# Performance work log

Hardware: AMD Instinct MI355X
Metric: run time of the kernel (lower is better)

## Reference

```python
import jax, jax.numpy as jnp
import numpy as np

LOG2PI = float(np.log(2.0 * np.pi))
T, DZ, DX = 512, 32, 32  # dx == dz so all quad forms stack homogeneously


def _spd(key, d):
    a = jax.random.normal(key, (d, d))
    return a @ a.T / d + jnp.eye(d)


def setup_inputs() -> dict:
    key = jax.random.key(0)
    k = jax.random.split(key, 17)
    return {
        "observations": jax.random.normal(k[0], (T, DX)),
        "m_prior_mean": jax.random.normal(k[1], (DZ,)),
        "m_prior_cov": _spd(k[2], DZ),
        "m_trans_w": 0.3 * jax.random.normal(k[3], (DZ, DZ)),
        "m_trans_b": jax.random.normal(k[4], (DZ,)),
        "m_trans_cov": _spd(k[5], DZ),
        "m_emis_w": 0.3 * jax.random.normal(k[6], (DX, DZ)),
        "m_emis_b": jax.random.normal(k[7], (DX,)),
        "m_emis_cov": _spd(k[8], DX),
        "v_prior_mean": jax.random.normal(k[9], (DZ,)),
        "v_prior_cov": _spd(k[10], DZ),
        "v_trans_w": 0.3 * jax.random.normal(k[11], (DZ, DZ)),
        "v_trans_b": jax.random.normal(k[12], (DZ,)),
        "v_trans_cov": _spd(k[13], DZ),
        "v_emis_w": 0.3 * jax.random.normal(k[14], (DX, DZ)),
        "v_emis_b": jax.random.normal(k[15], (DX,)),
        "v_emis_cov": _spd(k[16], DX),
    }


def _elbo(observations, m_prior_mean, m_prior_cov, m_trans_w, m_trans_b,
          m_trans_cov, m_emis_w, m_emis_b, m_emis_cov, v_prior_mean,
          v_prior_cov, v_trans_w, v_trans_b, v_trans_cov, v_emis_w,
          v_emis_b, v_emis_cov):
    Tn, dx = observations.shape
    dz = m_trans_cov.shape[0]
    I = jnp.eye(dz, dtype=observations.dtype)

    def logdet(M):
        return jnp.log(jnp.linalg.det(M))

    def cterm(dim, ld):  # -0.5*(dim*log(2pi) + log det)
        return -0.5 * (dim * LOG2PI + ld)

    m_trans_prec = jnp.linalg.inv(m_trans_cov)
    m_trans_ld = logdet(m_trans_cov)
    m_emis_prec = jnp.linalg.inv(m_emis_cov)
    m_emis_ld = logdet(m_emis_cov)
    v_trans_prec = jnp.linalg.inv(v_trans_cov)

    # ---- Kalman filter on the variational model ----
    def kf_update(m, P, y):
        S = v_emis_w @ P @ v_emis_w.T + v_emis_cov
        K = P @ v_emis_w.T @ jnp.linalg.inv(S)
        m2 = m + K @ (y - (v_emis_w @ m + v_emis_b))
        P2 = (I - K @ v_emis_w) @ P
        return m2, P2

    def kf_step(m, P, y):
        mp = v_trans_w @ m + v_trans_b
        Pp = v_trans_w @ P @ v_trans_w.T + v_trans_cov
        return kf_update(mp, Pp, y)

    # ---- stacked quad forms; list grows by 2 per step -> 2T slots ----
    N = 2 * Tn
    Om = jnp.zeros((N, dz, dz), observations.dtype)
    A = jnp.zeros((N, dz, dz), observations.dtype)
    b = jnp.zeros((N, dz), observations.dtype)
    # slot 0: emission/obs term at t=0
    Om = Om.at[0].set(-0.5 * m_emis_prec)
    A = A.at[0].set(m_emis_w)
    b = b.at[0].set(m_emis_b - observations[0])
    # slot 1: prior term
    Om = Om.at[1].set(-0.5 * jnp.linalg.inv(m_prior_cov))
    A = A.at[1].set(I)
    b = b.at[1].set(-m_prior_mean)

    fm, fP = kf_update(v_prior_mean, v_prior_cov, observations[0])
    c0 = cterm(dz, logdet(m_prior_cov)) + cterm(dx, m_emis_ld)

    def step(carry, xs):
        fm, fP, c, Om, A, b = carry
        t, y = xs
        # backward kernel from current filtering state
        fprec = jnp.linalg.inv(fP)
        common = v_trans_w.T @ v_trans_prec
        bcov = jnp.linalg.inv(common @ v_trans_w + fprec)
        bA = bcov @ common
        ba = bcov @ (fprec @ fm - common @ v_trans_b)
        # integrate all existing quad forms under the backward kernel
        # (zero slots contribute exactly 0, so no masking is needed)
        AbC = jnp.einsum('nij,jk->nik', A, bcov)
        c = c + jnp.sum(jnp.einsum('nab,nbc,nac->n', Om, AbC, A))
        A2 = jnp.einsum('nij,jk->nik', A, bA)
        b2 = jnp.einsum('nij,j->ni', A, ba) + b
        c = c + cterm(dx, m_emis_ld) + cterm(dz, m_trans_ld)
        # transition quad form expectation constant
        c = c - 0.5 * jnp.trace(m_trans_prec @ m_trans_w @ bcov @ m_trans_w.T)
        # append obs term (slot 2t) and transition term (slot 2t+1)
        Om2 = Om.at[2 * t].set(-0.5 * m_emis_prec).at[2 * t + 1].set(-0.5 * m_trans_prec)
        A2 = A2.at[2 * t].set(m_emis_w).at[2 * t + 1].set(m_trans_w @ bA - I)
        b2 = b2.at[2 * t].set(m_emis_b - y).at[2 * t + 1].set(m_trans_w @ ba + m_trans_b)
        # backward entropy constant + 0.5*dz
        c = c - cterm(dz, logdet(bcov)) + 0.5 * dz
        fm2, fP2 = kf_step(fm, fP, y)
        return (fm2, fP2, c, Om2, A2, b2), None

    ts = jnp.arange(1, Tn)
    (fm, fP, c, Om, A, b), _ = jax.lax.scan(
        step, (fm, fP, c0, Om, A, b), (ts, observations[1:]))

    # final expectations under the filtering distribution
    c = c - cterm(dz, logdet(fP))
    # trace(Omega @ A @ fP @ A)  -- note A (not A.T), faithful to the source
    tr = jnp.einsum('nab,nbc,cd,nda->n', Om, A, fP, A)
    cm = jnp.einsum('nij,j->ni', A, fm) + b
    qf = jnp.einsum('ni,nij,nj->n', cm, Om, cm)
    c = c + jnp.sum(tr) + jnp.sum(qf) + 0.5 * dz
    return c


def reference(observations, m_prior_mean, m_prior_cov, m_trans_w, m_trans_b,
              m_trans_cov, m_emis_w, m_emis_b, m_emis_cov, v_prior_mean,
              v_prior_cov, v_trans_w, v_trans_b, v_trans_cov, v_emis_w,
              v_emis_b, v_emis_cov):
    return _elbo(observations, m_prior_mean, m_prior_cov, m_trans_w,
                 m_trans_b, m_trans_cov, m_emis_w, m_emis_b, m_emis_cov,
                 v_prior_mean, v_prior_cov, v_trans_w, v_trans_b,
                 v_trans_cov, v_emis_w, v_emis_b, v_emis_cov)
```

## Files before the change

### kernel.cpp

```cpp
#include <hip/hip_runtime.h>
#include <math.h>

#define TT 512
#define CH 8
#define NCH 64
#define NB 128
#define ST 36
#define MS 1152
#define LOG2PI 1.8378770664093453

static_assert(TT == CH * NCH, "chunking");

enum : int {
  WS_X     = 0,
  WS_BCOV  = WS_X    + TT*1024,
  WS_BA    = WS_BCOV + TT*1024,
  WS_YT    = WS_BA   + TT*32,
  WS_MTP   = WS_YT   + TT*32,
  WS_MEP   = WS_MTP + 1024,
  WS_MPP   = WS_MEP + 1024,
  WS_QI    = WS_MPP + 1024,
  WS_RI    = WS_QI  + 1024,
  WS_P0I   = WS_RI  + 1024,
  WS_QIW   = WS_P0I + 1024,
  WS_CW    = WS_QIW + 1024,
  WS_HTRI  = WS_CW  + 1024,
  WS_HTRIH = WS_HTRI+ 1024,
  WS_TQ    = WS_HTRIH+1024,
  WS_EM    = WS_TQ  + 1024,
  WS_EML   = WS_EM  + 1024,
  WS_LAM0CW= WS_EML + 1024,
  WS_QHC   = WS_LAM0CW + 1024,
  WS_C1    = WS_QHC + 1024,
  WS_EMM   = WS_C1  + 1024,
  WS_S1    = WS_EMM + 1024,
  WS_FPT   = WS_S1  + 1024,
  WS_ETA0  = WS_FPT + 1024,
  WS_CTB   = WS_ETA0 + 32,
  WS_QIVTB = WS_CTB + 32,
  WS_FMT   = WS_QIVTB + 32,
  WS_ETAF  = WS_FMT + 32,
  WS_LDS3  = WS_ETAF + 32,
  WS_DACC  = WS_LDS3 + 4,
  WS_Z512  = WS_DACC + 8,
  WS_OPS   = WS_Z512 + 1024,
  WS_GBAR  = WS_OPS + 6*3072,
  WS_ETA_A = WS_GBAR + 64,
  WS_ETA_B = WS_ETA_A + NCH*1056,
  WS_CEA   = WS_ETA_B + NCH*1056,
  WS_CEB   = WS_CEA + NCH*2048,
  WS_END   = WS_CEB + NCH*2048
};
enum : int { WS_GEA = WS_CEA, WS_GEB = WS_CEB };
static_assert(WS_DACC % 2 == 0, "double alignment");

__device__ __forceinline__ float rlane(float v, int l) {
  return __uint_as_float(__builtin_amdgcn_readlane(__float_as_uint(v), l));
}
__device__ __forceinline__ float dot4(const float4 a, const float4 b) {
  return a.x*b.x + a.y*b.y + a.z*b.z + a.w*b.w;
}

__device__ __forceinline__ double gj_inv32(float a[32]) {
  double pp = 1.0;
#pragma unroll
  for (int p = 0; p < 32; ++p) {
    const float piv = rlane(a[p], p);
    pp *= (double)piv;
    const float sc = a[p] * (1.0f / piv);
#pragma unroll
    for (int r = 0; r < 32; ++r) {
      if (r != p) a[r] -= rlane(a[r], p) * sc;
    }
    a[p] = sc;
  }
  return pp;
}

__device__ __forceinline__ double wave_inv36(float* M, int tid) {
  float a[32]; const int cc = tid & 31;
#pragma unroll
  for (int r = 0; r < 32; ++r)
    a[r] = (tid < 32) ? M[r*ST + cc] : ((r == tid - 32) ? 1.f : 0.f);
  const double pp = gj_inv32(a);
  if (tid >= 32) {
    const int c2 = tid - 32;
#pragma unroll
// ... 83 lines not shown
  const int ri = tid >> 3, j4 = (tid & 7) * 4;
  float4 acc = *(const float4*)(Base + ri*ST + j4);
#pragma unroll 8
  for (int k = 0; k < 32; ++k) {
    const float a = A[ri*ST + k];
    const float4 b = *(const float4*)(B + k*ST + j4);
    acc.x -= a*b.x; acc.y -= a*b.y; acc.z -= a*b.z; acc.w -= a*b.w;
  }
  *(float4*)(C + ri*ST + j4) = acc;
}
__device__ __forceinline__ void mm_tp(const float* A, const float* B, float* C, int tid) {
  const int ri = tid >> 3, j4 = (tid & 7) * 4;
  float4 acc = {0.f,0.f,0.f,0.f};
#pragma unroll 8
  for (int k = 0; k < 32; ++k) {
    const float a = A[k*ST + ri];
    const float4 b = *(const float4*)(B + k*ST + j4);
    acc.x += a*b.x; acc.y += a*b.y; acc.z += a*b.z; acc.w += a*b.w;
  }
  *(float4*)(C + ri*ST + j4) = acc;
}
__device__ __forceinline__ void mm_tp_addL(const float* A, const float* B,
                                           const float* AddL, float* C, int tid) {
  const int ri = tid >> 3, j4 = (tid & 7) * 4;
  float4 acc = *(const float4*)(AddL + ri*ST + j4);
#pragma unroll 8
  for (int k = 0; k < 32; ++k) {
    const float a = A[k*ST + ri];
    const float4 b = *(const float4*)(B + k*ST + j4);
    acc.x += a*b.x; acc.y += a*b.y; acc.z += a*b.z; acc.w += a*b.w;
  }
  *(float4*)(C + ri*ST + j4) = acc;
}
__device__ __forceinline__ void mm_tp_addg(const float* A, const float* B,
                                           const float* __restrict__ gAdd,
                                           float* C, int tid) {
  const int ri = tid >> 3, j4 = (tid & 7) * 4;
  float4 acc = *(const float4*)(gAdd + ri*32 + j4);
#pragma unroll 8
  for (int k = 0; k < 32; ++k) {
    const float a = A[k*ST + ri];
    const float4 b = *(const float4*)(B + k*ST + j4);
    acc.x += a*b.x; acc.y += a*b.y; acc.z += a*b.z; acc.w += a*b.w;
  }
  *(float4*)(C + ri*ST + j4) = acc;
}

__device__ __forceinline__ void gridbar(unsigned* bars, int idx) {
  __syncthreads();
  if (threadIdx.x == 0) {
    __threadfence();
    __hip_atomic_fetch_add(&bars[idx], 1u, __ATOMIC_RELEASE, __HIP_MEMORY_SCOPE_AGENT);
    while (__hip_atomic_load(&bars[idx], __ATOMIC_ACQUIRE, __HIP_MEMORY_SCOPE_AGENT)
           < (unsigned)NB)
      __builtin_amdgcn_s_sleep(2);
  }
  __syncthreads();
}

__device__ void dev_k2(const float* __restrict__ obs, const float* __restrict__ vpm,
                       const float* __restrict__ vtw, const float* __restrict__ vtb,
                       const float* __restrict__ vew, const float* __restrict__ veb,
                       const float* __restrict__ mtw, const float* __restrict__ mew,
                       float* __restrict__ ws, int tid) {
  const int j = tid & 31, r0 = tid >> 5;
#pragma unroll
  for (int m = 0; m < 4; ++m) {
    const int ri = r0 + 8*m;
    float s1 = 0.f, s2 = 0.f, s3 = 0.f, s4 = 0.f;
    for (int k = 0; k < 32; ++k) {
      s1 += ws[WS_QI  + ri*32 + k] * vtw[k*32 + j];
      s2 += vew[k*32 + ri] * ws[WS_RI + k*32 + j];
      s3 += ws[WS_MTP + ri*32 + k] * mtw[k*32 + j];
      s4 += ws[WS_MEP + ri*32 + k] * mew[k*32 + j];
    }
    ws[WS_QIW + ri*32 + j] = s1;
    ws[WS_HTRI + ri*32 + j] = s2;
    ws[WS_FPT + ri*32 + j] = s3;
    ws[WS_EML + ri*32 + j] = -0.5f * s4;
  }
  __syncthreads();
#pragma unroll
  for (int m = 0; m < 4; ++m) {
    const int ri = r0 + 8*m;
    float s1 = 0.f, s2 = 0.f, s3 = 0.f, s4 = 0.f;
    for (int k = 0; k < 32; ++k) {
      s1 += vtw[k*32 + ri] * ws[WS_QIW + k*32 + j];
      s2 += ws[WS_HTRI + ri*32 + k] * vew[k*32 + j];
// ... 5 lines not shown
    ws[WS_LAM0CW + ri*32 + j] = ws[WS_P0I + ri*32 + j] + s1 + s2;
    ws[WS_QHC    + ri*32 + j] = ws[WS_QI  + ri*32 + j] + s1 + s2;
    ws[WS_TQ + ri*32 + j] = s3;
    ws[WS_EM + ri*32 + j] = s4;
    ws[WS_S1 + ri*32 + j] = s4 - 0.5f * ws[WS_MPP + ri*32 + j];
    ws[WS_C1 + ri*32 + j] = ws[WS_FPT + j*32 + ri];
    ws[WS_EMM + ri*32 + j] = s4 - 0.5f * ws[WS_MTP + ri*32 + j];
  }
  if (tid < 32) {
    float s1 = 0.f, s2 = 0.f, s3 = 0.f;
    for (int k = 0; k < 32; ++k) {
      s1 += ws[WS_QIW + k*32 + tid] * vtb[k];
      s2 += ws[WS_P0I + tid*32 + k] * vpm[k]
          + ws[WS_HTRI + tid*32 + k] * (obs[k] - veb[k]);
      s3 += ws[WS_QI + tid*32 + k] * vtb[k];
    }
    ws[WS_CTB + tid] = s1;
    ws[WS_ETA0 + tid] = s2;
    ws[WS_QIVTB + tid] = s3;
  }
  __syncthreads();
  if (tid == 0) {
    const double ldmt = (double)ws[WS_LDS3 + 0];
    const double ldme = (double)ws[WS_LDS3 + 1];
    const double ldmp = (double)ws[WS_LDS3 + 2];
    const double ct_me = -0.5 * (32.0 * LOG2PI + ldme);
    const double ct_mt = -0.5 * (32.0 * LOG2PI + ldmt);
    const double ct_mp = -0.5 * (32.0 * LOG2PI + ldmp);
    double c = ct_mp + ct_me;
    c += (double)(TT - 1) * (ct_me + ct_mt + 0.5 * 32.0 * LOG2PI + 16.0);
    c += 0.5 * 32.0 * LOG2PI + 16.0;
    ((double*)(ws + WS_DACC))[0] = c;
  }
}

__device__ void dev_compose(float* __restrict__ ws, float* sm, int tid) {
  float *Kc = sm,      *Ac = sm+MS,   *Gc = sm+2*MS;
  float *Kn = sm+3*MS, *An = sm+4*MS, *Gn = sm+5*MS;
  float *Mi = sm+6*MS, *V1 = sm+7*MS, *Wm = sm+8*MS;
  stage_mat(ws + WS_QHC, Kc, tid);
  stage_mat(ws + WS_QIW, Ac, tid);
  for (int e = tid; e < MS; e += 256) Gc[e] = 0.f;
  __syncthreads();
  for (int d = 0; d < 8; ++d) {
    for (int e = tid; e < MS; e += 256) Mi[e] = Kc[e] + Gc[e];
    __syncthreads();
    if (tid < 64) wave_inv36(Mi, tid);
    __syncthreads();
    mm_rr(Ac, Mi, V1, tid);
    mm_tp(Ac, Mi, Wm, tid);
    __syncthreads();
    mm_rr_sub(V1, Ac, Kc, Kn, tid);
    mm_p(V1, Ac, An, tid);
    mm_p_sub(Wm, Ac, Gc, Gn, tid);
    __syncthreads();
    float* tp;
    tp=Kc; Kc=Kn; Kn=tp;  tp=Ac; Ac=An; An=tp;  tp=Gc; Gc=Gn; Gn=tp;
    if (d >= 2) {
      float* op = ws + WS_OPS + (d-2)*3072;
      destage_mat(Kc, op, tid);
      destage_mat(Ac, op + 1024, tid);
      destage_mat(Gc, op + 2048, tid);
    }
  }
}

__device__ void dev_keta_a(float* __restrict__ ws, float* sm, int tid, int c) {
  float *Aa = sm, *Ab = sm+MS, *Xl = sm+2*MS, *bb = sm+3*MS;
  const int t1 = CH*c + 1;
  stage_mat(ws + WS_X + t1*1024, Aa, tid);
  if (tid < 32) bb[tid] = ws[WS_YT + t1*32 + tid];
  __syncthreads();
  float *Acur = Aa, *Anew = Ab; int pb = 0;
  for (int t = t1 + 1; t <= t1 + CH - 1; ++t) {
    stage_mat(ws + WS_X + t*1024, Xl, tid);
    __syncthreads();
    mm_p(Xl, Acur, Anew, tid);
    if (tid < 32) {
      float s = ws[WS_YT + t*32 + tid];
      for (int k = 0; k < 32; ++k) s += Xl[tid*ST+k] * bb[pb*32 + k];
      bb[(pb^1)*32 + tid] = s;
    }
    __syncthreads();
    float* tp = Acur; Acur = Anew; Anew = tp; pb ^= 1;
  }
  float* dst = ws + WS_ETA_A + (c+1)*1056;
  destage_mat(Acur, dst, tid);
  if (tid < 32) dst[1024 + tid] = bb[pb*32 + tid];
}

__device__ void dev_eta_lvl4(float* __restrict__ ws, float* sm,
                             int inoff, int outoff, int step, int tid, int c) {
  const float* in = ws + inoff;
  float* out = ws + outoff;
  float *AR0 = sm, *AR1 = sm+MS, *A0 = sm+2*MS;
  float *bv = sm+3*MS;
  float *b0 = bv + 64;
  stage_mat(in + c*1056, AR0, tid);
  if (tid < 32) bv[tid] = in[c*1056 + 1024 + tid];
  __syncthreads();
  float *AR = AR0, *At = AR1; int pb = 0;
  for (int kk = 1; kk <= 3; ++kk) {
    const int idx = c - kk*step;
    if (idx < 0) break;
    stage_mat(in + idx*1056, A0, tid);
    if (tid < 32) b0[tid] = in[idx*1056 + 1024 + tid];
    __syncthreads();
    mm_p(AR, A0, At, tid);
    if (tid < 32) {
      float s = bv[pb*32 + tid];
      for (int k = 0; k < 32; ++k) s += AR[tid*ST+k] * b0[k];
      bv[(pb^1)*32 + tid] = s;
    }
    __syncthreads();
    float* tp = AR; AR = At; At = tp; pb ^= 1;
  }
  destage_mat(AR, out + c*1056, tid);
  if (tid < 32) out[c*1056 + 1024 + tid] = bv[pb*32 + tid];
}

__device__ void dev_keta_b(float* __restrict__ ws, float* sm, int tid, int c) {
  float *Ap = sm, *Bl = sm+MS, *Xl = sm+2*MS, *zeta = sm+3*MS, *zn = zeta+32;
  const int nst = (c == NCH-1) ? CH-1 : CH;
  stage_mat(ws + WS_ETA_B + c*1056, Ap, tid);
  __syncthreads();
  if (tid < 32) {
    float s = ws[WS_ETA_B + c*1056 + 1024 + tid];
    for (int k = 0; k < 32; ++k)
      s += Ap[tid*ST+k] * (ws[WS_ETA0 + k] - ws[WS_CTB + k]);
    zeta[tid] = s;
  }
  __syncthreads();
  for (int i = 0; i < nst; ++i) {
    const int t = CH*c + 1 + i;
    stage_mat(ws + WS_BCOV + t*1024, Bl, tid);
    stage_mat(ws + WS_X + t*1024, Xl, tid);
    __syncthreads();
    if (tid < 32) {
      float s = 0.f;
      for (int k = 0; k < 32; ++k) s += Bl[tid*ST+k] * zeta[k];
      ws[WS_BA + t*32 + tid] = s;
    } else if (tid < 64) {
      const int i2 = tid - 32;
      float s = ws[WS_YT + t*32 + i2];
      for (int k = 0; k < 32; ++k) s += Xl[i2*ST+k] * zeta[k];
      zn[i2] = s;
    }
    __syncthreads();
    if (tid < 32) zeta[tid] = zn[tid];
    __syncthreads();
  }
  if (c == NCH-1 && tid < 32)
    ws[WS_ETAF + tid] = zeta[tid] + ws[WS_CTB + tid];
}

__device__ void dev_ksa(float* __restrict__ ws, float* sm, int tid, int c) {
  float *BTa=sm,      *BTb=sm+MS,   *Ka=sm+2*MS,  *Kb=sm+3*MS,
        *Tk=sm+4*MS,  *XC1=sm+5*MS, *Xl=sm+6*MS,  *KmTQ=sm+7*MS,
        *TQl=sm+8*MS, *EMMl=sm+9*MS,*C1l=sm+10*MS;
  const int t1 = CH*c + 1, t2 = CH*c + CH;
  const int j = tid & 31, r0 = tid >> 5;
  stage_mat(ws + WS_TQ, TQl, tid);
  stage_mat(ws + WS_EMM, EMMl, tid);
  stage_mat(ws + WS_C1, C1l, tid);
  for (int e = tid; e < MS; e += 256) {
// ... 4 lines not shown
  __syncthreads();
  float *BTc = BTa, *BTn = BTb, *Kc = Ka, *Kn = Kb;
  for (int t = t1; t <= t2; ++t) {
    stage_mat(ws + WS_X + t*1024, Xl, tid);
    for (int e = tid; e < MS; e += 256) KmTQ[e] = Kc[e] - 0.5f * TQl[e];
    __syncthreads();
    mm_rr(BTc, Xl, BTn, tid);
    mm_rr(Xl, KmTQ, Tk, tid);
    mm_p(Xl, C1l, XC1, tid);
    __syncthreads();
    {
      float4 xb[8];
#pragma unroll
      for (int kk = 0; kk < 8; ++kk) xb[kk] = *(const float4*)(Xl + j*ST + 4*kk);
#pragma unroll
      for (int m = 0; m < 4; ++m) {
        const int ri = r0 + 8*m;
        float s = 0.f;
#pragma unroll
        for (int kk = 0; kk < 8; ++kk)
          s += dot4(*(const float4*)(Tk + ri*ST + 4*kk), xb[kk]);
        Kn[ri*ST+j] = s + 0.5f*(XC1[ri*ST+j] + XC1[j*ST+ri]) + EMMl[ri*ST+j];
      }
    }
    __syncthreads();
    float* tp = BTc; BTc = BTn; BTn = tp;
    tp = Kc; Kc = Kn; Kn = tp;
  }
  float* dst = ws + WS_CEA + (c+1)*2048;
  destage_mat(BTc, dst, tid);
  destage_mat(Kc, dst + 1024, tid);
}

__device__ void dev_ks_lvl4(float* __restrict__ ws, float* sm,
                            int inoff, int outoff, int step, int tid, int c) {
  const float* in = ws + inoff;
  float* out = ws + outoff;
  float *BT0=sm,      *BT1=sm+MS,   *K0=sm+2*MS, *K1=sm+3*MS,
        *BTo=sm+4*MS, *Ko=sm+5*MS,  *tmp=sm+6*MS;
  stage_mat(in + c*2048, BT0, tid);
  stage_mat(in + c*2048 + 1024, K0, tid);
  __syncthreads();
  float *BTR = BT0, *BTt = BT1, *KR = K0, *Kt = K1;
  for (int kk = 1; kk <= 3; ++kk) {
    const int idx = c - kk*step;
    if (idx < 0) break;
    stage_mat(in + idx*2048, BTo, tid);
    stage_mat(in + idx*2048 + 1024, Ko, tid);
    __syncthreads();
    mm_p(Ko, BTR, tmp, tid);
    mm_p(BTo, BTR, BTt, tid);
    __syncthreads();
    mm_tp_addL(BTR, tmp, KR, Kt, tid);
    __syncthreads();
    float* tp = BTR; BTR = BTt; BTt = tp;
    tp = KR; KR = Kt; Kt = tp;
  }
  destage_mat(BTR, out + c*2048, tid);
  destage_mat(KR, out + c*2048 + 1024, tid);
}

__device__ void dev_ksc(float* __restrict__ ws, float* sm, float* red,
                        int tid, int c) {
  float *TQl=sm,    *EMMl=sm+MS,  *C1l=sm+2*MS, *BTP=sm+3*MS, *T1=sm+4*MS,
        *S=sm+5*MS, *SmTQ=sm+6*MS,*Xl=sm+7*MS,  *Bcl=sm+8*MS, *XC1=sm+9*MS;
  const int j = tid & 31, r0 = tid >> 5;
  stage_mat(ws + WS_TQ, TQl, tid);
  stage_mat(ws + WS_EMM, EMMl, tid);
  stage_mat(ws + WS_C1, C1l, tid);
  stage_mat(ws + WS_CEB + c*2048, BTP, tid);
  stage_mat(ws + WS_S1, SmTQ, tid);
  __syncthreads();
  mm_p(SmTQ, BTP, T1, tid);
  __syncthreads();
  mm_tp_addg(BTP, T1, ws + WS_CEB + c*2048 + 1024, S, tid);
  __syncthreads();
  double accd = 0.0;
  for (int i = 0; i < CH; ++i) {
    const int t = CH*c + 1 + i;
    if (t >= TT) break;
    stage_mat(ws + WS_X + t*1024, Xl, tid);
    stage_mat(ws + WS_BCOV + t*1024, Bcl, tid);
#pragma unroll
    for (int m = 0; m < 4; ++m) {
      const int ri = r0 + 8*m;
      SmTQ[ri*ST+j] = S[ri*ST+j] - 0.5f * TQl[ri*ST+j];
    }
    __syncthreads();
    float part = 0.f;
#pragma unroll
    for (int m = 0; m < 4; ++m) {
      const int ri = r0 + 8*m;
      part += SmTQ[ri*ST+j] * Bcl[ri*ST+j];
    }
    const float r2 = block_reduce(part, red, tid);
    if (tid == 0) accd += (double)r2;
    mm_rr(Xl, SmTQ, T1, tid);
    mm_p(Xl, C1l, XC1, tid);
    __syncthreads();
    {
      float4 xb[8];
#pragma unroll
      for (int kk = 0; kk < 8; ++kk) xb[kk] = *(const float4*)(Xl + j*ST + 4*kk);
#pragma unroll
      for (int m = 0; m < 4; ++m) {
        const int ri = r0 + 8*m;
        float s = 0.f;
#pragma unroll
        for (int kk = 0; kk < 8; ++kk)
          s += dot4(*(const float4*)(T1 + ri*ST + 4*kk), xb[kk]);
        S[ri*ST+j] = s + 0.5f*(XC1[ri*ST+j] + XC1[j*ST+ri]) + EMMl[ri*ST+j];
      }
    }
    __syncthreads();
  }
  if (tid == 0) atomicAdd(((double*)(ws + WS_DACC)) + 2, accd);
}

__device__ void dev_kga(float* __restrict__ ws, float* sm, int tid, int c) {
  float *ATa = sm, *ATb = sm+MS, *Xl = sm+2*MS, *bb = sm+3*MS;
  const int t1 = CH*c + 1;
  const int t2 = (CH*c + CH < TT) ? CH*c + CH : TT - 1;
  stage_mat(ws + WS_X + t2*1024, ATa, tid);
  if (tid < 32) bb[tid] = ws[WS_BA + t2*32 + tid];
  __syncthreads();
  float *ATc = ATa, *ATn = ATb;
  int pb = 0;
  for (int t = t2 - 1; t >= t1; --t) {
    stage_mat(ws + WS_X + t*1024, Xl, tid);
    __syncthreads();
    mm_p(ATc, Xl, ATn, tid);
    if (tid < 32) {
      float s = ws[WS_BA + t*32 + tid];
      for (int k = 0; k < 32; ++k) s += Xl[k*ST+tid] * bb[pb*32 + k];
      bb[(pb^1)*32 + tid] = s;
    }
    __syncthreads();
    float* tp = ATc; ATc = ATn; ATn = tp; pb ^= 1;
  }
  float* dst = ws + WS_GEA + (c-1)*1056;
  destage_mat(ATc, dst, tid);
  if (tid < 32) dst[1024 + tid] = bb[pb*32 + tid];
}

__device__ void dev_kg_lvl4(float* __restrict__ ws, float* sm,
                            int inoff, int outoff, int step, int tid, int c) {
  const float* in = ws + inoff;
  float* out = ws + outoff;
  float *AR0 = sm, *AR1 = sm+MS, *ATl = sm+2*MS;
  float *bv = sm+3*MS, *bl = bv + 64;
  stage_mat(in + c*1056, AR0, tid);
  if (tid < 32) bv[tid] = in[c*1056 + 1024 + tid];
  __syncthreads();
  float *AR = AR0, *At = AR1; int pb = 0;
  for (int kk = 1; kk <= 3; ++kk) {
    const int idx = c + kk*step;
    if (idx > NCH - 1) break;
    stage_mat(in + idx*1056, ATl, tid);
    if (tid < 32) bl[tid] = in[idx*1056 + 1024 + tid];
    __syncthreads();
    mm_p(ATl, AR, At, tid);
    if (tid < 32) {
      float s = bv[pb*32 + tid];
      for (int k = 0; k < 32; ++k) s += AR[k*ST+tid] * bl[k];
      bv[(pb^1)*32 + tid] = s;
    }
    __syncthreads();
    float* tp = AR; AR = At; At = tp; pb ^= 1;
  }
  destage_mat(AR, out + c*1056, tid);
  if (tid < 32) out[c*1056 + 1024 + tid] = bv[pb*32 + tid];
}

__device__ void dev_kgb(const float* __restrict__ obs, const float* __restrict__ mpm,
                        const float* __restrict__ mtw, const float* __restrict__ mtb,
                        const float* __restrict__ mew, const float* __restrict__ meb,
                        float* __restrict__ ws, float* sm, float* red, int tid, int c) {
  float *ATa=sm,      *ATb=sm+MS,    *Xl=sm+2*MS,  *Y1=sm+3*MS,  *Y2=sm+4*MS,
        *Jb=sm+5*MS,  *M2T=sm+6*MS,  *mewl=sm+7*MS,*EmLl=sm+8*MS,
        *fPl=sm+9*MS, *Mtpl=sm+10*MS,*Mepl=sm+11*MS,*mtwl=sm+12*MS;
  float *vec = sm + 13*MS;
  float *fml=vec, *mebl=vec+32, *mtbl=vec+64, *mpml=vec+96, *yl=vec+128,
        *bal=vec+160, *gv=vec+192, *cme=vec+224, *cmo=vec+256, *bv=vec+288;
  const int j = tid & 31, r0 = tid >> 5;
  stage_mat(mew, mewl, tid);
  stage_mat(ws + WS_EML, EmLl, tid);
  stage_mat(ws + WS_FPT, fPl, tid);
  stage_mat(ws + WS_MTP, Mtpl, tid);
  stage_mat(ws + WS_MEP, Mepl, tid);
  stage_mat(mtw, mtwl, tid);
  stage_mat(ws + WS_GEB + c*1056, ATa, tid);
  if (tid < 32) {
    fml[tid] = ws[WS_FMT + tid];
    mebl[tid] = meb[tid]; mtbl[tid] = mtb[tid]; mpml[tid] = mpm[tid];
    bv[tid] = ws[WS_GEB + c*1056 + 1024 + tid];
  }
  __syncthreads();
  float *ATc = ATa, *ATo = ATb;
  int bc = 0;
  double accd = 0.0;
  for (int s = CH*c + CH - 1; s >= CH*c; --s) {
    if (s < TT-1) stage_mat(ws + WS_X + (s+1)*1024, Xl, tid);
    if (s == 0)   stage_mat(ws + WS_MPP, Jb, tid);
    if (tid < 32) {
      yl[tid] = obs[s*32 + tid];
      if (s >= 1) bal[tid] = ws[WS_BA + s*32 + tid];
    }
    __syncthreads();
    if (s < TT-1) {
      mm_p(ATc, Xl, ATo, tid);
      if (tid < 32) {
        float v = ws[WS_BA + (s+1)*32 + tid];
        for (int k = 0; k < 32; ++k) v += Xl[k*ST+tid] * bv[bc*32 + k];
        bv[(bc^1)*32 + tid] = v;
      }
    }
    __syncthreads();
    const float* AT = (s < TT-1) ? ATo : ATc;
    const float* bl = (s < TT-1) ? (bv + (bc^1)*32) : (bv + bc*32);
    mm_rr(mewl, AT, Y1, tid);
    mm_rr(EmLl, AT, Y2, tid);
    if (s >= 1) {
      const float* Xg = ws + WS_X + s*1024;
      float4 xg[8];
#pragma unroll
      for (int kk = 0; kk < 8; ++kk) xg[kk] = *(const float4*)(Xg + j*32 + 4*kk);
#pragma unroll
      for (int m = 0; m < 4; ++m) {
        const int ri = r0 + 8*m;
        float v = 0.f;
#pragma unroll
        for (int kk = 0; kk < 8; ++kk)
// ... 22 lines not shown
      }
      cmo[tid] = s2v;
    }
    __syncthreads();
    const float* M2Tp = (s >= 1) ? M2T : AT;
    const float* Mqp  = (s >= 1) ? Mtpl : Jb;
    float4 fb[8], m2b[8];
#pragma unroll
    for (int kk = 0; kk < 8; ++kk) {
      fb[kk]  = *(const float4*)(fPl + j*ST + 4*kk);
      m2b[kk] = *(const float4*)(M2Tp + j*ST + 4*kk);
    }
    float part = 0.f;
#pragma unroll
    for (int m = 0; m < 4; ++m) {
      const int ri = r0 + 8*m;
      float y3 = 0.f, e2 = 0.f, e1 = 0.f;
#pragma unroll
      for (int kk = 0; kk < 8; ++kk) {
        y3 += dot4(*(const float4*)(Y2 + ri*ST + 4*kk), fb[kk]);
        e2 += dot4(fb[kk], *(const float4*)(M2Tp + ri*ST + 4*kk));
        e1 += dot4(*(const float4*)(Mqp + ri*ST + 4*kk), m2b[kk]);
      }
      part += y3 * Y1[j*ST+ri]
            - 0.5f * e1 * e2
            - 0.5f * cme[ri] * Mepl[ri*ST+j] * cme[j]
            - 0.5f * cmo[ri] * Mqp[ri*ST+j] * cmo[j];
    }
    const float r2 = block_reduce(part, red, tid);
    if (tid == 0) accd += (double)r2;
    if (s < TT-1) { float* tp = ATc; ATc = ATo; ATo = tp; bc ^= 1; }
    __syncthreads();
  }
  if (tid == 0) atomicAdd(((double*)(ws + WS_DACC)) + 3, accd);
}

__global__ __launch_bounds__(128) void k0_init(float* __restrict__ ws) {
  const int tid = threadIdx.x;
  if (tid < 64) ((unsigned*)(ws + WS_GBAR))[tid] = 0u;
  if (tid == 64) ((double*)(ws + WS_DACC))[1] = 0.0;
  if (tid == 65) ((double*)(ws + WS_DACC))[2] = 0.0;
  if (tid == 66) ((double*)(ws + WS_DACC))[3] = 0.0;
}

__global__ __launch_bounds__(256) void mega(
    const float* __restrict__ obs, const float* __restrict__ mpm,
    const float* __restrict__ mpc, const float* __restrict__ mtw,
    const float* __restrict__ mtb, const float* __restrict__ mtc,
    const float* __restrict__ mew, const float* __restrict__ meb,
    const float* __restrict__ mec, const float* __restrict__ vpm,
    const float* __restrict__ vpc, const float* __restrict__ vtw,
    const float* __restrict__ vtb, const float* __restrict__ vtc,
    const float* __restrict__ vew, const float* __restrict__ veb,
    const float* __restrict__ vcc, float* __restrict__ ws,
    float* __restrict__ out) {
  __shared__ __align__(16) float sm[15360];
  __shared__ float red[4];
  const int tid = threadIdx.x, blk = blockIdx.x;
  unsigned* bars = (unsigned*)(ws + WS_GBAR);
  int bix = 0;

  if (blk < 6) {
    const float* src = blk==0?mtc : blk==1?mec : blk==2?mpc : blk==3?vtc : blk==4?vcc : vpc;
    float* dst = ws + (blk==0?WS_MTP : blk==1?WS_MEP : blk==2?WS_MPP :
                       blk==3?WS_QI  : blk==4?WS_RI  : WS_P0I);
    if (tid < 64) {
      float a[32]; const int cc = tid & 31;
#pragma unroll
      for (int r = 0; r < 32; ++r)
        a[r] = (tid < 32) ? src[r*32 + cc] : ((r == tid - 32) ? 1.f : 0.f);
      const double pp = gj_inv32(a);
      if (tid >= 32) {
        const int c2 = tid - 32;
#pragma unroll
        for (int r = 0; r < 32; ++r) dst[r*32 + c2] = a[r];
      }
      if (tid == 0 && blk < 3) ws[WS_LDS3 + blk] = (float)log(pp);
    }
  }
  gridbar(bars, bix++);

  if (blk == 0) dev_k2(obs, vpm, vtw, vtb, vew, veb, mtw, mew, ws, tid);
  gridbar(bars, bix++);

  if (blk == 0) {
    dev_compose(ws, sm, tid);
  } else if (blk <= NCH) {
    const int tb = blk - 1;
    const int t = tb*CH + (tid >> 5), i = tid & 31;
    float s = ws[WS_QIVTB + i] - ws[WS_CTB + i];
    for (int k = 0; k < 32; ++k)
      s += ws[WS_HTRI + i*32 + k] * (obs[t*32 + k] - veb[k]);
    ws[WS_YT + t*32 + i] = s;
  }
  gridbar(bars, bix++);

  if (blk < NCH) {
    float *Zl=sm, *Mi=sm+MS, *Aol=sm+2*MS, *V1=sm+3*MS;
    float *Bcv=sm+4*MS, *Xs=sm+5*MS, *QiWl=sm+6*MS, *QHCl=sm+7*MS;
    const int c = blk;
    stage_mat(ws + WS_LAM0CW, Zl, tid);
    stage_mat(ws + WS_QIW, QiWl, tid);
    stage_mat(ws + WS_QHC, QHCl, tid);
    __syncthreads();
    for (int k = 0; k < 6; ++k) {
      if (!((c >> k) & 1)) continue;
      const float* OP = ws + WS_OPS + k*3072;
      {
        const int r = tid >> 3, c4 = (tid & 7) * 4;
        const float4 g = *(const float4*)(OP + 2048 + r*32 + c4);
        float4 z = *(const float4*)(Zl + r*ST + c4);
        z.x += g.x; z.y += g.y; z.z += g.z; z.w += g.w;
        *(float4*)(Mi + r*ST + c4) = z;
      }
      stage_mat(OP + 1024, Aol, tid);
      __syncthreads();
      if (tid < 64) wave_inv36(Mi, tid);
      __syncthreads();
      mm_rr(Aol, Mi, V1, tid);
      __syncthreads();
      mm_rr_subg(V1, Aol, OP, Zl, tid);
      __syncthreads();
    }
    const int nst = (c == NCH-1) ? CH-1 : CH;
    double acc = 0.0;
    for (int i = 0; i < nst; ++i) {
      const int t = CH*c + 1 + i;
      if (tid < 64) {
        float a[32]; const int cc = tid & 31;
#pragma unroll
        for (int r = 0; r < 32; ++r)
          a[r] = (tid < 32) ? Zl[r*ST+cc] : ((r == tid - 32) ? 1.f : 0.f);
        const double pp = gj_inv32(a);
        if (tid >= 32) {
          const int c2 = tid - 32;
#pragma unroll
          for (int r = 0; r < 32; ++r) {
            Bcv[r*ST + c2] = a[r];
            ws[WS_BCOV + t*1024 + r*32 + c2] = a[r];
          }
        }
        if (tid == 0) acc += -log(pp);
      }
      __syncthreads();
      mm_rr(QiWl, Bcv, Xs, tid);
      __syncthreads();
      destage_mat(Xs, ws + WS_X + t*1024, tid);
      mm_rr_sub(Xs, QiWl, QHCl, Zl, tid);
      __syncthreads();
    }
    if (c == NCH-1) destage_mat(Zl, ws + WS_Z512, tid);
    if (tid == 0) atomicAdd(((double*)(ws + WS_DACC)) + 1, acc);
  }
  gridbar(bars, bix++);

  if (blk < NCH) {
    if (blk < NCH-1) {
      dev_keta_a(ws, sm, tid, blk);
    } else {
      for (int e = tid; e < 1056; e += 256)
        ws[WS_ETA_A + e] = (e < 1024 && ((e >> 5) == (e & 31))) ? 1.f : 0.f;
    }
  } else {
    const int c = blk - NCH;
    if (c < NCH-1) {
      dev_ksa(ws, sm, tid, c);
    } else {
      for (int e = tid; e < 2048; e += 256)
        ws[WS_CEA + e] = (e < 1024 && ((e >> 5) == (e & 31))) ? 1.f : 0.f;
    }
  }
  gridbar(bars, bix++);

  {
    const int steps[3] = {1, 4, 16};
#pragma unroll
    for (int L = 0; L < 3; ++L) {
      const int inA = (L & 1) == 0;
      if (blk < NCH) {
        dev_eta_lvl4(ws, sm, inA ? WS_ETA_A : WS_ETA_B,
                     inA ? WS_ETA_B : WS_ETA_A, steps[L], tid, blk);
      } else {
        dev_ks_lvl4(ws, sm, inA ? WS_CEA : WS_CEB,
                    inA ? WS_CEB : WS_CEA, steps[L], tid, blk - NCH);
      }
      gridbar(bars, bix++);
    }
  }

  if (blk < NCH) {
    dev_keta_b(ws, sm, tid, blk);
    __threadfence();
    __syncthreads();
    if (blk == 0) {
      for (int e = tid; e < 1056; e += 256)
        ws[WS_GEA + (NCH-1)*1056 + e] =
            (e < 1024 && ((e >> 5) == (e & 31))) ? 1.f : 0.f;
    } else {
      dev_kga(ws, sm, tid, blk);
    }
  } else {
    dev_ksc(ws, sm, red, tid, blk - NCH);
  }
  gridbar(bars, bix++);

  {
    const int steps[3] = {1, 4, 16};
#pragma unroll
    for (int L = 0; L < 3; ++L) {
      const int inA = (L & 1) == 0;
      if (blk < NCH) {
        dev_kg_lvl4(ws, sm, inA ? WS_GEA : WS_GEB,
                    inA ? WS_GEB : WS_GEA, steps[L], tid, blk);
      } else if (L == 0 && blk == NB-1) {
        if (tid < 64) {
          float a[32]; const int cc = tid & 31;
#pragma unroll
          for (int r = 0; r < 32; ++r) {
            const float v = ws[WS_Z512 + r*32 + cc] - ws[WS_CW + r*32 + cc];
            a[r] = (tid < 32) ? v : ((r == tid - 32) ? 1.f : 0.f);
          }
          const double pp = gj_inv32(a);
          if (tid >= 32) {
            const int c2 = tid - 32;
            float fmv = 0.f;
#pragma unroll
            for (int r = 0; r < 32; ++r) {
              ws[WS_FPT + r*32 + c2] = a[r];
              fmv += a[r] * ws[WS_ETAF + r];
            }
            ws[WS_FMT + c2] = fmv;
          }
          if (tid == 0) {
            double* d = (double*)(ws + WS_DACC);
            d[1] = 0.5 * (d[1] + (-log(pp)));
          }
        }
      }
      gridbar(bars, bix++);
    }
  }

  if (blk < NCH) dev_kgb(obs, mpm, mtw, mtb, mew, meb, ws, sm, red, tid, blk);
  gridbar(bars, bix++);

  if (blk == 0 && tid == 0) {
    const double* d = (const double*)(ws + WS_DACC);
    out[0] = (float)(d[0] + d[1] + d[2] + d[3]);
  }
}

extern "C" void kernel_launch(void* const* d_in, const int* in_sizes, int n_in,
                              void* d_out, int out_size, void* d_ws, size_t ws_size,
                              hipStream_t stream) {
  (void)in_sizes; (void)n_in; (void)out_size; (void)ws_size;
  const float* obs = (const float*)d_in[0];
  const float* mpm = (const float*)d_in[1];
  const float* mpc = (const float*)d_in[2];
  const float* mtw = (const float*)d_in[3];
  const float* mtb = (const float*)d_in[4];
  const float* mtc = (const float*)d_in[5];
  const float* mew = (const float*)d_in[6];
  const float* meb = (const float*)d_in[7];
  const float* mec = (const float*)d_in[8];
  const float* vpm = (const float*)d_in[9];
  const float* vpc = (const float*)d_in[10];
  const float* vtw = (const float*)d_in[11];
  const float* vtb = (const float*)d_in[12];
  const float* vtc = (const float*)d_in[13];
  const float* vew = (const float*)d_in[14];
  const float* veb = (const float*)d_in[15];
  const float* vcc = (const float*)d_in[16];
  float* ws  = (float*)d_ws;
  float* out = (float*)d_out;

  k0_init<<<1, 128, 0, stream>>>(ws);
  mega<<<NB, 256, 0, stream>>>(obs, mpm, mpc, mtw, mtb, mtc, mew, meb, mec,
                               vpm, vpc, vtw, vtb, vtc, vew, veb, vcc, ws, out);
}
```

Before: 618.5 us.

## Cut grid barriers with hierarchical barrier, radix-8 scans, and per-block partial sums

Replaces the three radix-4 parallel-scan levels (step 1,4,16) with one radix-8 level plus a stride-8 second pass folded into the following consumer stages, dropping four grid barriers in each scan. Merges the k2 and compose stages and moves the Y-transform onto idle blocks, removing two more barriers. The grid barrier becomes a two-level group/global tree with separate cache-line-spaced counters. Double atomicAdd accumulations become per-block partial slots reduced by a final shuffle. The cost is more serial matmuls per block in each scan stage, traded for fewer global synchronisations.

```diff
diff --git a/kernel.cpp b/kernel.cpp
--- a/kernel.cpp
+++ b/kernel.cpp
@@ -5,6 +5,8 @@
 #define CH 8
 #define NCH 64
 #define NB 128
+#define NGRP 8
+#define GSZ (NB/NGRP)
 #define ST 36
 #define MS 1152
 #define LOG2PI 1.8378770664093453
@@ -45,14 +47,14 @@
   WS_Z512  = WS_DACC + 8,
   WS_OPS   = WS_Z512 + 1024,
   WS_GBAR  = WS_OPS + 6*3072,
-  WS_ETA_A = WS_GBAR + 64,
+  WS_PART  = WS_GBAR + 4352,
+  WS_ETA_A = WS_PART + 416,
   WS_ETA_B = WS_ETA_A + NCH*1056,
   WS_CEA   = WS_ETA_B + NCH*1056,
   WS_CEB   = WS_CEA + NCH*2048,
   WS_END   = WS_CEB + NCH*2048
 };
-enum : int { WS_GEA = WS_CEA, WS_GEB = WS_CEB };
-static_assert(WS_DACC % 2 == 0, "double alignment");
+static_assert(WS_DACC % 2 == 0 && WS_PART % 2 == 0, "double alignment");
 
 __device__ __forceinline__ float rlane(float v, int l) {
   return __uint_as_float(__builtin_amdgcn_readlane(__float_as_uint(v), l));
@@ -202,28 +204,29 @@
   }
   *(float4*)(C + ri*ST + j4) = acc;
 }
-__device__ __forceinline__ void mm_tp_addg(const float* A, const float* B,
-                                           const float* __restrict__ gAdd,
-                                           float* C, int tid) {
-  const int ri = tid >> 3, j4 = (tid & 7) * 4;
-  float4 acc = *(const float4*)(gAdd + ri*32 + j4);
-#pragma unroll 8
-  for (int k = 0; k < 32; ++k) {
-    const float a = A[k*ST + ri];
-    const float4 b = *(const float4*)(B + k*ST + j4);
-    acc.x += a*b.x; acc.y += a*b.y; acc.z += a*b.z; acc.w += a*b.w;
-  }
-  *(float4*)(C + ri*ST + j4) = acc;
-}
-
-__device__ __forceinline__ void gridbar(unsigned* bars, int idx) {
+
+__device__ __forceinline__ void gridbar(unsigned* base, int idx, int blk) {
   __syncthreads();
   if (threadIdx.x == 0) {
+    const int g = blk & (NGRP-1);
+    unsigned* lcl  = base + idx*128 + g*16;
+    unsigned* go   = base + 2048 + idx*128 + g*16;
+    unsigned* glob = base + 4096 + idx*16;
     __threadfence();
-    __hip_atomic_fetch_add(&bars[idx], 1u, __ATOMIC_RELEASE, __HIP_MEMORY_SCOPE_AGENT);
-    while (__hip_atomic_load(&bars[idx], __ATOMIC_ACQUIRE, __HIP_MEMORY_SCOPE_AGENT)
-           < (unsigned)NB)
-      __builtin_amdgcn_s_sleep(2);
+    __hip_atomic_fetch_add(lcl, 1u, __ATOMIC_RELEASE, __HIP_MEMORY_SCOPE_AGENT);
+    if (blk < NGRP) {
+      while (__hip_atomic_load(lcl, __ATOMIC_ACQUIRE, __HIP_MEMORY_SCOPE_AGENT)
+             < (unsigned)GSZ)
+        __builtin_amdgcn_s_sleep(1);
+      __hip_atomic_fetch_add(glob, 1u, __ATOMIC_RELEASE, __HIP_MEMORY_SCOPE_AGENT);
+      while (__hip_atomic_load(glob, __ATOMIC_ACQUIRE, __HIP_MEMORY_SCOPE_AGENT)
+             < (unsigned)NGRP)
+        __builtin_amdgcn_s_sleep(1);
+      __hip_atomic_store(go, 1u, __ATOMIC_RELEASE, __HIP_MEMORY_SCOPE_AGENT);
+    } else {
+      while (__hip_atomic_load(go, __ATOMIC_ACQUIRE, __HIP_MEMORY_SCOPE_AGENT) == 0u)
+        __builtin_amdgcn_s_sleep(1);
+    }
   }
   __syncthreads();
 }
@@ -295,6 +298,7 @@
     c += 0.5 * 32.0 * LOG2PI + 16.0;
     ((double*)(ws + WS_DACC))[0] = c;
   }
+  __syncthreads();
 }
 
 __device__ void dev_compose(float* __restrict__ ws, float* sm, int tid) {
@@ -352,19 +356,17 @@
   if (tid < 32) dst[1024 + tid] = bb[pb*32 + tid];
 }
 
-__device__ void dev_eta_lvl4(float* __restrict__ ws, float* sm,
-                             int inoff, int outoff, int step, int tid, int c) {
-  const float* in = ws + inoff;
-  float* out = ws + outoff;
+__device__ void dev_eta_lvl8(float* __restrict__ ws, float* sm, int tid, int c) {
+  const float* in = ws + WS_ETA_A;
+  float* out = ws + WS_ETA_B;
   float *AR0 = sm, *AR1 = sm+MS, *A0 = sm+2*MS;
-  float *bv = sm+3*MS;
-  float *b0 = bv + 64;
+  float *bv = sm+3*MS, *b0 = bv + 64;
   stage_mat(in + c*1056, AR0, tid);
   if (tid < 32) bv[tid] = in[c*1056 + 1024 + tid];
   __syncthreads();
   float *AR = AR0, *At = AR1; int pb = 0;
-  for (int kk = 1; kk <= 3; ++kk) {
-    const int idx = c - kk*step;
+  for (int kk = 1; kk <= 7; ++kk) {
+    const int idx = c - kk;
     if (idx < 0) break;
     stage_mat(in + idx*1056, A0, tid);
     if (tid < 32) b0[tid] = in[idx*1056 + 1024 + tid];
@@ -383,17 +385,37 @@
 }
 
 __device__ void dev_keta_b(float* __restrict__ ws, float* sm, int tid, int c) {
-  float *Ap = sm, *Bl = sm+MS, *Xl = sm+2*MS, *zeta = sm+3*MS, *zn = zeta+32;
+  float *A_0 = sm, *A_1 = sm+MS, *A_2 = sm+2*MS;
+  float *bb = sm+3*MS;
+  stage_mat(ws + WS_ETA_B + c*1056, A_0, tid);
+  if (tid < 32) bb[tid] = ws[WS_ETA_B + c*1056 + 1024 + tid];
+  __syncthreads();
+  float *AR = A_0, *Ax = A_1; int pb = 0;
+  for (int kk = 1; kk <= 7; ++kk) {
+    const int idx = c - 8*kk;
+    if (idx < 0) break;
+    stage_mat(ws + WS_ETA_B + idx*1056, A_2, tid);
+    if (tid < 32) bb[64 + tid] = ws[WS_ETA_B + idx*1056 + 1024 + tid];
+    __syncthreads();
+    mm_p(AR, A_2, Ax, tid);
+    if (tid < 32) {
+      float s = bb[pb*32 + tid];
+      for (int k = 0; k < 32; ++k) s += AR[tid*ST+k] * bb[64+k];
+      bb[(pb^1)*32 + tid] = s;
+    }
+    __syncthreads();
+    float* tp = AR; AR = Ax; Ax = tp; pb ^= 1;
+  }
+  float *zeta = bb + 96, *zn = bb + 128;
+  if (tid < 32) {
+    float s = bb[pb*32 + tid];
+    for (int k = 0; k < 32; ++k)
+      s += AR[tid*ST+k] * (ws[WS_ETA0 + k] - ws[WS_CTB + k]);
+    zeta[tid] = s;
+  }
+  __syncthreads();
+  float *Bl = A_0, *Xl = A_1;
   const int nst = (c == NCH-1) ? CH-1 : CH;
-  stage_mat(ws + WS_ETA_B + c*1056, Ap, tid);
-  __syncthreads();
-  if (tid < 32) {
-    float s = ws[WS_ETA_B + c*1056 + 1024 + tid];
-    for (int k = 0; k < 32; ++k)
-      s += Ap[tid*ST+k] * (ws[WS_ETA0 + k] - ws[WS_CTB + k]);
-    zeta[tid] = s;
-  }
-  __syncthreads();
   for (int i = 0; i < nst; ++i) {
     const int t = CH*c + 1 + i;
     stage_mat(ws + WS_BCOV + t*1024, Bl, tid);
@@ -464,18 +486,17 @@
   destage_mat(Kc, dst + 1024, tid);
 }
 
-__device__ void dev_ks_lvl4(float* __restrict__ ws, float* sm,
-                            int inoff, int outoff, int step, int tid, int c) {
-  const float* in = ws + inoff;
-  float* out = ws + outoff;
-  float *BT0=sm,      *BT1=sm+MS,   *K0=sm+2*MS, *K1=sm+3*MS,
-        *BTo=sm+4*MS, *Ko=sm+5*MS,  *tmp=sm+6*MS;
+__device__ void dev_ks_lvl8(float* __restrict__ ws, float* sm, int tid, int c) {
+  const float* in = ws + WS_CEA;
+  float* out = ws + WS_CEB;
+  float *BT0=sm, *BT1=sm+MS, *K0=sm+2*MS, *K1=sm+3*MS,
+        *BTo=sm+4*MS, *Ko=sm+5*MS, *tmp=sm+6*MS;
   stage_mat(in + c*2048, BT0, tid);
   stage_mat(in + c*2048 + 1024, K0, tid);
   __syncthreads();
-  float *BTR = BT0, *BTt = BT1, *KR = K0, *Kt = K1;
-  for (int kk = 1; kk <= 3; ++kk) {
-    const int idx = c - kk*step;
+  float *BTR=BT0, *BTt=BT1, *KR=K0, *Kt=K1;
+  for (int kk = 1; kk <= 7; ++kk) {
+    const int idx = c - kk;
     if (idx < 0) break;
     stage_mat(in + idx*2048, BTo, tid);
     stage_mat(in + idx*2048 + 1024, Ko, tid);
@@ -494,18 +515,38 @@
 
 __device__ void dev_ksc(float* __restrict__ ws, float* sm, float* red,
                         int tid, int c) {
-  float *TQl=sm,    *EMMl=sm+MS,  *C1l=sm+2*MS, *BTP=sm+3*MS, *T1=sm+4*MS,
-        *S=sm+5*MS, *SmTQ=sm+6*MS,*Xl=sm+7*MS,  *Bcl=sm+8*MS, *XC1=sm+9*MS;
+  float *BT0=sm, *BT1=sm+MS, *K0=sm+2*MS, *K1=sm+3*MS,
+        *BTo=sm+4*MS, *Ko=sm+5*MS, *tmp=sm+6*MS;
+  stage_mat(ws + WS_CEB + c*2048, BT0, tid);
+  stage_mat(ws + WS_CEB + c*2048 + 1024, K0, tid);
+  __syncthreads();
+  float *BTR=BT0, *BTt=BT1, *KR=K0, *Kt=K1;
+  for (int kk = 1; kk <= 7; ++kk) {
+    const int idx = c - 8*kk;
+    if (idx < 0) break;
+    stage_mat(ws + WS_CEB + idx*2048, BTo, tid);
+    stage_mat(ws + WS_CEB + idx*2048 + 1024, Ko, tid);
+    __syncthreads();
+    mm_p(Ko, BTR, tmp, tid);
+    mm_p(BTo, BTR, BTt, tid);
+    __syncthreads();
+    mm_tp_addL(BTR, tmp, KR, Kt, tid);
+    __syncthreads();
+    float* tp = BTR; BTR = BTt; BTt = tp;
+    tp = KR; KR = Kt; Kt = tp;
+  }
+  float *TQl=sm+7*MS, *EMMl=sm+8*MS, *C1l=sm+9*MS,
+        *S=sm+10*MS, *SmTQ=sm+11*MS, *XC1=sm+12*MS;
+  float *T1=tmp, *Xl=BTo, *Bcl=Ko;
   const int j = tid & 31, r0 = tid >> 5;
   stage_mat(ws + WS_TQ, TQl, tid);
   stage_mat(ws + WS_EMM, EMMl, tid);
   stage_mat(ws + WS_C1, C1l, tid);
-  stage_mat(ws + WS_CEB + c*2048, BTP, tid);
   stage_mat(ws + WS_S1, SmTQ, tid);
   __syncthreads();
-  mm_p(SmTQ, BTP, T1, tid);
-  __syncthreads();
-  mm_tp_addg(BTP, T1, ws + WS_CEB + c*2048 + 1024, S, tid);
+  mm_p(SmTQ, BTR, T1, tid);
+  __syncthreads();
+  mm_tp_addL(BTR, T1, KR, S, tid);
   __syncthreads();
   double accd = 0.0;
   for (int i = 0; i < CH; ++i) {
@@ -546,7 +587,7 @@
     }
     __syncthreads();
   }
-  if (tid == 0) atomicAdd(((double*)(ws + WS_DACC)) + 2, accd);
+  if (tid == 0) ((double*)(ws + WS_PART))[64 + c] = accd;
 }
 
 __device__ void dev_kga(float* __restrict__ ws, float* sm, int tid, int c) {
@@ -570,23 +611,22 @@
     __syncthreads();
     float* tp = ATc; ATc = ATn; ATn = tp; pb ^= 1;
   }
-  float* dst = ws + WS_GEA + (c-1)*1056;
+  float* dst = ws + WS_CEA + (c-1)*1056;
   destage_mat(ATc, dst, tid);
   if (tid < 32) dst[1024 + tid] = bb[pb*32 + tid];
 }
 
-__device__ void dev_kg_lvl4(float* __restrict__ ws, float* sm,
-                            int inoff, int outoff, int step, int tid, int c) {
-  const float* in = ws + inoff;
-  float* out = ws + outoff;
+__device__ void dev_kg_lvl8(float* __restrict__ ws, float* sm, int tid, int c) {
+  const float* in = ws + WS_CEA;
+  float* out = ws + WS_CEB;
   float *AR0 = sm, *AR1 = sm+MS, *ATl = sm+2*MS;
   float *bv = sm+3*MS, *bl = bv + 64;
   stage_mat(in + c*1056, AR0, tid);
   if (tid < 32) bv[tid] = in[c*1056 + 1024 + tid];
   __syncthreads();
   float *AR = AR0, *At = AR1; int pb = 0;
-  for (int kk = 1; kk <= 3; ++kk) {
-    const int idx = c + kk*step;
+  for (int kk = 1; kk <= 7; ++kk) {
+    const int idx = c + kk;
     if (idx > NCH - 1) break;
     stage_mat(in + idx*1056, ATl, tid);
     if (tid < 32) bl[tid] = in[idx*1056 + 1024 + tid];
@@ -621,15 +661,30 @@
   stage_mat(ws + WS_MTP, Mtpl, tid);
   stage_mat(ws + WS_MEP, Mepl, tid);
   stage_mat(mtw, mtwl, tid);
-  stage_mat(ws + WS_GEB + c*1056, ATa, tid);
+  stage_mat(ws + WS_CEB + c*1056, ATa, tid);
   if (tid < 32) {
     fml[tid] = ws[WS_FMT + tid];
     mebl[tid] = meb[tid]; mtbl[tid] = mtb[tid]; mpml[tid] = mpm[tid];
-    bv[tid] = ws[WS_GEB + c*1056 + 1024 + tid];
+    bv[tid] = ws[WS_CEB + c*1056 + 1024 + tid];
   }
   __syncthreads();
   float *ATc = ATa, *ATo = ATb;
   int bc = 0;
+  for (int kk = 1; kk <= 7; ++kk) {
+    const int idx = c + 8*kk;
+    if (idx > NCH - 1) break;
+    stage_mat(ws + WS_CEB + idx*1056, Xl, tid);
+    if (tid < 32) bal[tid] = ws[WS_CEB + idx*1056 + 1024 + tid];
+    __syncthreads();
+    mm_p(Xl, ATc, ATo, tid);
+    if (tid < 32) {
+      float s = bv[bc*32 + tid];
+      for (int k = 0; k < 32; ++k) s += ATc[k*ST+tid] * bal[k];
+      bv[(bc^1)*32 + tid] = s;
+    }
+    __syncthreads();
+    float* tp = ATc; ATc = ATo; ATo = tp; bc ^= 1;
+  }
   double accd = 0.0;
   for (int s = CH*c + CH - 1; s >= CH*c; --s) {
     if (s < TT-1) stage_mat(ws + WS_X + (s+1)*1024, Xl, tid);
@@ -718,15 +773,12 @@
     if (s < TT-1) { float* tp = ATc; ATc = ATo; ATo = tp; bc ^= 1; }
     __syncthreads();
   }
-  if (tid == 0) atomicAdd(((double*)(ws + WS_DACC)) + 3, accd);
-}
-
-__global__ __launch_bounds__(128) void k0_init(float* __restrict__ ws) {
-  const int tid = threadIdx.x;
-  if (tid < 64) ((unsigned*)(ws + WS_GBAR))[tid] = 0u;
-  if (tid == 64) ((double*)(ws + WS_DACC))[1] = 0.0;
-  if (tid == 65) ((double*)(ws + WS_DACC))[2] = 0.0;
-  if (tid == 66) ((double*)(ws + WS_DACC))[3] = 0.0;
+  if (tid == 0) ((double*)(ws + WS_PART))[128 + c] = accd;
+}
+
+__global__ __launch_bounds__(256) void k0_init(float* __restrict__ ws) {
+  unsigned* b = (unsigned*)(ws + WS_GBAR);
+  for (int e = threadIdx.x; e < 4352; e += 256) b[e] = 0u;
 }
 
 __global__ __launch_bounds__(256) void mega(
@@ -744,6 +796,7 @@
   __shared__ float red[4];
   const int tid = threadIdx.x, blk = blockIdx.x;
   unsigned* bars = (unsigned*)(ws + WS_GBAR);
+  double* P = (double*)(ws + WS_PART);
   int bix = 0;
 
   if (blk < 6) {
@@ -764,22 +817,13 @@
       if (tid == 0 && blk < 3) ws[WS_LDS3 + blk] = (float)log(pp);
     }
   }
-  gridbar(bars, bix++);
-
-  if (blk == 0) dev_k2(obs, vpm, vtw, vtb, vew, veb, mtw, mew, ws, tid);
-  gridbar(bars, bix++);
+  gridbar(bars, bix++, blk);
 
   if (blk == 0) {
+    dev_k2(obs, vpm, vtw, vtb, vew, veb, mtw, mew, ws, tid);
     dev_compose(ws, sm, tid);
-  } else if (blk <= NCH) {
-    const int tb = blk - 1;
-    const int t = tb*CH + (tid >> 5), i = tid & 31;
-    float s = ws[WS_QIVTB + i] - ws[WS_CTB + i];
-    for (int k = 0; k < 32; ++k)
-      s += ws[WS_HTRI + i*32 + k] * (obs[t*32 + k] - veb[k]);
-    ws[WS_YT + t*32 + i] = s;
-  }
-  gridbar(bars, bix++);
+  }
+  gridbar(bars, bix++, blk);
 
   if (blk < NCH) {
     float *Zl=sm, *Mi=sm+MS, *Aol=sm+2*MS, *V1=sm+3*MS;
@@ -836,9 +880,16 @@
       __syncthreads();
     }
     if (c == NCH-1) destage_mat(Zl, ws + WS_Z512, tid);
-    if (tid == 0) atomicAdd(((double*)(ws + WS_DACC)) + 1, acc);
-  }
-  gridbar(bars, bix++);
+    if (tid == 0) P[blk] = acc;
+  } else {
+    const int tb = blk - NCH;
+    const int t = tb*CH + (tid >> 5), i = tid & 31;
+    float s = ws[WS_QIVTB + i] - ws[WS_CTB + i];
+    for (int k = 0; k < 32; ++k)
+      s += ws[WS_HTRI + i*32 + k] * (obs[t*32 + k] - veb[k]);
+    ws[WS_YT + t*32 + i] = s;
+  }
+  gridbar(bars, bix++, blk);
 
   if (blk < NCH) {
     if (blk < NCH-1) {
@@ -856,23 +907,11 @@
         ws[WS_CEA + e] = (e < 1024 && ((e >> 5) == (e & 31))) ? 1.f : 0.f;
     }
   }
-  gridbar(bars, bix++);
-
-  {
-    const int steps[3] = {1, 4, 16};
-#pragma unroll
-    for (int L = 0; L < 3; ++L) {
-      const int inA = (L & 1) == 0;
-      if (blk < NCH) {
-        dev_eta_lvl4(ws, sm, inA ? WS_ETA_A : WS_ETA_B,
-                     inA ? WS_ETA_B : WS_ETA_A, steps[L], tid, blk);
-      } else {
-        dev_ks_lvl4(ws, sm, inA ? WS_CEA : WS_CEB,
-                    inA ? WS_CEB : WS_CEA, steps[L], tid, blk - NCH);
-      }
-      gridbar(bars, bix++);
-    }
-  }
+  gridbar(bars, bix++, blk);
+
+  if (blk < NCH) dev_eta_lvl8(ws, sm, tid, blk);
+  else           dev_ks_lvl8(ws, sm, tid, blk - NCH);
+  gridbar(bars, bix++, blk);
 
   if (blk < NCH) {
     dev_keta_b(ws, sm, tid, blk);
@@ -880,7 +919,7 @@
     __syncthreads();
     if (blk == 0) {
       for (int e = tid; e < 1056; e += 256)
-        ws[WS_GEA + (NCH-1)*1056 + e] =
+        ws[WS_CEA + (NCH-1)*1056 + e] =
             (e < 1024 && ((e >> 5) == (e & 31))) ? 1.f : 0.f;
     } else {
       dev_kga(ws, sm, tid, blk);
@@ -888,51 +927,45 @@
   } else {
     dev_ksc(ws, sm, red, tid, blk - NCH);
   }
-  gridbar(bars, bix++);
-
-  {
-    const int steps[3] = {1, 4, 16};
-#pragma unroll
-    for (int L = 0; L < 3; ++L) {
-      const int inA = (L & 1) == 0;
-      if (blk < NCH) {
-        dev_kg_lvl4(ws, sm, inA ? WS_GEA : WS_GEB,
-                    inA ? WS_GEB : WS_GEA, steps[L], tid, blk);
-      } else if (L == 0 && blk == NB-1) {
-        if (tid < 64) {
-          float a[32]; const int cc = tid & 31;
-#pragma unroll
-          for (int r = 0; r < 32; ++r) {
-            const float v = ws[WS_Z512 + r*32 + cc] - ws[WS_CW + r*32 + cc];
-            a[r] = (tid < 32) ? v : ((r == tid - 32) ? 1.f : 0.f);
-          }
-          const double pp = gj_inv32(a);
-          if (tid >= 32) {
-            const int c2 = tid - 32;
-            float fmv = 0.f;
-#pragma unroll
-            for (int r = 0; r < 32; ++r) {
-              ws[WS_FPT + r*32 + c2] = a[r];
-              fmv += a[r] * ws[WS_ETAF + r];
-            }
-            ws[WS_FMT + c2] = fmv;
-          }
-          if (tid == 0) {
-            double* d = (double*)(ws + WS_DACC);
-            d[1] = 0.5 * (d[1] + (-log(pp)));
-          }
+  gridbar(bars, bix++, blk);
+
+  if (blk < NCH) {
+    dev_kg_lvl8(ws, sm, tid, blk);
+  } else if (blk == NCH) {
+    if (tid < 64) {
+      float a[32]; const int cc = tid & 31;
+#pragma unroll
+      for (int r = 0; r < 32; ++r) {
+        const float v = ws[WS_Z512 + r*32 + cc] - ws[WS_CW + r*32 + cc];
+        a[r] = (tid < 32) ? v : ((r == tid - 32) ? 1.f : 0.f);
+      }
+      const double pp = gj_inv32(a);
+      if (tid >= 32) {
+        const int c2 = tid - 32;
+        float fmv = 0.f;
+#pragma unroll
+        for (int r = 0; r < 32; ++r) {
+          ws[WS_FPT + r*32 + c2] = a[r];
+          fmv += a[r] * ws[WS_ETAF + r];
         }
-      }
-      gridbar(bars, bix++);
-    }
-  }
+        ws[WS_FMT + c2] = fmv;
+      }
+      if (tid == 0) P[192] = -log(pp);
+    }
+  }
+  gridbar(bars, bix++, blk);
 
   if (blk < NCH) dev_kgb(obs, mpm, mtw, mtb, mew, meb, ws, sm, red, tid, blk);
-  gridbar(bars, bix++);
-
-  if (blk == 0 && tid == 0) {
-    const double* d = (const double*)(ws + WS_DACC);
-    out[0] = (float)(d[0] + d[1] + d[2] + d[3]);
+  gridbar(bars, bix++, blk);
+
+  if (blk == 0 && tid < 64) {
+    double v = 0.5 * P[tid] + P[64 + tid] + P[128 + tid];
+#pragma unroll
+    for (int m = 32; m >= 1; m >>= 1) v += __shfl_xor(v, m, 64);
+    if (tid == 0) {
+      const double* d = (const double*)(ws + WS_DACC);
+      out[0] = (float)(v + d[0] + 0.5 * P[192]);
+    }
   }
 }
 
@@ -960,7 +993,7 @@
   float* ws  = (float*)d_ws;
   float* out = (float*)d_out;
 
-  k0_init<<<1, 128, 0, stream>>>(ws);
+  k0_init<<<1, 256, 0, stream>>>(ws);
   mega<<<NB, 256, 0, stream>>>(obs, mpm, mpc, mtw, mtb, mtc, mew, meb, mec,
                                vpm, vpc, vtw, vtb, vtc, vew, veb, vcc, ws, out);
 }
```

Result: faster. 606.3 us (-2.0%).
